# Kernel optimization log

Measured on AMD Instinct MI355X. Metric: run time of the kernel, lower is better.

## Reference

```python
import jax, jax.numpy as jnp
import numpy as np

H, QP, VP, D, DP = 4, 4, 4, 128, 64
DH = D // H


def setup_inputs() -> dict:
    key = jax.random.key(0)
    ks = jax.random.split(key, 16)
    B, L = 1, 1024
    w_c0 = float(np.log(np.e - 1.0))
    inp = {
        'single': jax.random.normal(ks[0], (B, L, D), jnp.float32),
        'pair': jax.random.normal(ks[1], (B, L, L, DP), jnp.float32),
        'T': jax.random.normal(ks[2], (B, L, 4, 4), jnp.float32),
        'w_C': jnp.full((H,), w_c0, jnp.float32),
        'ln_g': jnp.ones((D,), jnp.float32),
        'ln_b': jnp.zeros((D,), jnp.float32),
        'Wq': jax.random.normal(ks[3], (D, H * DH), jnp.float32) * 0.05,
        'Wk': jax.random.normal(ks[4], (D, H * DH), jnp.float32) * 0.05,
        'Wv': jax.random.normal(ks[5], (D, H * DH), jnp.float32) * 0.05,
        'Wqpt': jax.random.normal(ks[6], (D, H * QP * 3), jnp.float32) * 0.05,
        'Wkpt': jax.random.normal(ks[7], (D, H * QP * 3), jnp.float32) * 0.05,
        'Wvpt': jax.random.normal(ks[8], (D, H * VP * 3), jnp.float32) * 0.05,
        'Wb': jax.random.normal(ks[9], (DP, H), jnp.float32) * 0.05,
        'Wout': jax.random.normal(ks[10], (H * (DH + DP + VP * 3 + VP), D), jnp.float32) * 0.05,
        'b_out': jnp.zeros((D,), jnp.float32),
    }
    return inp


def _layernorm(x, g, b, eps=1e-5):
    x32 = x.astype(jnp.float32)
    mu = x32.mean(-1, keepdims=True)
    var = ((x32 - mu) ** 2).mean(-1, keepdims=True)
    return ((x32 - mu) * jax.lax.rsqrt(var + eps) * g + b).astype(x.dtype)


def reference(single, pair, T, w_C, ln_g, ln_b, Wq, Wk, Wv, Wqpt, Wkpt, Wvpt, Wb, Wout, b_out):
    B, L, Dm = single.shape
    scale_attn = DH ** (-0.5)
    z = _layernorm(single, ln_g, ln_b)
    Q = (z @ Wq).reshape(B, L, H, DH)
    K = (z @ Wk).reshape(B, L, H, DH)
    V = (z @ Wv).reshape(B, L, H, DH)
    Q_pt = (z @ Wqpt).reshape(B, L, H, QP, 3)
    K_pt = (z @ Wkpt).reshape(B, L, H, QP, 3)
    V_pt = (z @ Wvpt).reshape(B, L, H, VP, 3)
    R = T[..., :3, :3]   # [B,L,3,3]
    t = T[..., :3, 3]    # [B,L,3]
    # global-frame points: R @ p + t
    Q_g = jnp.einsum('blxy,blhpy->blhpx', R, Q_pt) + t[:, :, None, None, :]
    K_g = jnp.einsum('blxy,blhpy->blhpx', R, K_pt) + t[:, :, None, None, :]
    V_g = jnp.einsum('blxy,blhpy->blhpx', R, V_pt) + t[:, :, None, None, :]
    # scalar QK score [B,H,L,L]
    s_attn = jnp.einsum('bihd,bjhd->bhij', Q, K) * scale_attn
    # pair bias [B,H,L,L]
    b_attn = jnp.einsum('bijc,ch->bhij', pair, Wb)
    # squared point distance [B,H,L,L]
    diff = Q_g[:, :, None] - K_g[:, None]          # [B,L,L,H,QP,3]
    d2 = jnp.moveaxis((diff ** 2).sum((-1, -2)), -1, 1)
    w_pt = jax.nn.softplus(w_C)[None, :, None, None]
    attn = jax.nn.softmax(s_attn + b_attn - 0.5 * w_pt * d2, axis=-1)
    # scalar values [B,L,H*DH]
    o_s = jnp.einsum('bhij,bjhd->bihd', attn, V).reshape(B, L, H * DH)
    # point values aggregated in global frame then mapped back: R^T (p - t)
    o_pt_g = jnp.einsum('bhij,bjhpx->bihpx', attn, V_g)
    o_pt = jnp.einsum('blyx,blhpy->blhpx', R, o_pt_g - t[:, :, None, None, :])
    o_pt_n = jnp.sqrt((o_pt ** 2).sum(-1))
    # pair aggregation [B,L,H*DP]
    o_pair = jnp.einsum('bhij,bijc->bihc', attn, pair).reshape(B, L, H * DP)
    out = jnp.concatenate([o_s, o_pair, o_pt.reshape(B, L, -1), o_pt_n.reshape(B, L, -1)], axis=-1)
    return single + out @ Wout + b_out
```

## Files before the change

kernel.cpp:

```cpp
#include <hip/hip_runtime.h>
#include <math.h>

#define L_SEQ 1024
#define DM 128

#define OFF_KHAT 0
#define OFF_QHAT (L_SEQ * 192)
#define OFF_V    (OFF_QHAT + L_SEQ * 192)
#define OFF_VG   (OFF_V + L_SEQ * DM)

typedef __attribute__((address_space(1))) const void* gas_t;
typedef __attribute__((address_space(3))) void* las_t;

__device__ __forceinline__ void async16(const float4* g, float4* l) {
    __builtin_amdgcn_global_load_lds((gas_t)g, (las_t)l, 16, 0, 0);
}

__global__ __launch_bounds__(256) void ipa_prep(
    const float* __restrict__ single, const float* __restrict__ T,
    const float* __restrict__ w_C, const float* __restrict__ ln_g, const float* __restrict__ ln_b,
    const float* __restrict__ Wq, const float* __restrict__ Wk, const float* __restrict__ Wv,
    const float* __restrict__ Wqpt, const float* __restrict__ Wkpt, const float* __restrict__ Wvpt,
    float* __restrict__ ws)
{
    __shared__ float z_lds[128];
    __shared__ float proj[528];
    __shared__ float qg[4][4][3];
    __shared__ float kg[4][4][3];
    __shared__ float cq[4], ck[4];

    const int t = threadIdx.x;
    const int i = blockIdx.x;

    if (t < 64) {
        float x0 = single[i*DM + t];
        float x1 = single[i*DM + 64 + t];
        float s = x0 + x1, s2 = x0*x0 + x1*x1;
        #pragma unroll
        for (int off = 1; off < 64; off <<= 1) { s += __shfl_xor(s, off); s2 += __shfl_xor(s2, off); }
        float mu = s * 0.0078125f;
        float var = s2 * 0.0078125f - mu*mu;
        float rs = rsqrtf(var + 1e-5f);
        z_lds[t]      = (x0 - mu) * rs * ln_g[t]      + ln_b[t];
        z_lds[t + 64] = (x1 - mu) * rs * ln_g[t + 64] + ln_b[t + 64];
    }
    __syncthreads();

    for (int cc = t; cc < 528; cc += 256) {
        const float* W; int col, ncol;
        if (cc < 128)      { W = Wq;   col = cc;       ncol = 128; }
        else if (cc < 256) { W = Wk;   col = cc - 128; ncol = 128; }
        else if (cc < 384) { W = Wv;   col = cc - 256; ncol = 128; }
        else if (cc < 432) { W = Wqpt; col = cc - 384; ncol = 48;  }
        else if (cc < 480) { W = Wkpt; col = cc - 432; ncol = 48;  }
        else               { W = Wvpt; col = cc - 480; ncol = 48;  }
        float a = 0.f;
        #pragma unroll 8
        for (int k = 0; k < 128; ++k)
            a = fmaf(z_lds[k], W[k*ncol + col], a);
        proj[cc] = a;
    }
    __syncthreads();

    if (t < 16) {
        int h = t >> 2, p = t & 3;
        float R[3][3], tt[3];
        #pragma unroll
        for (int x = 0; x < 3; ++x) {
            #pragma unroll
            for (int y = 0; y < 3; ++y) R[x][y] = T[i*16 + x*4 + y];
            tt[x] = T[i*16 + x*4 + 3];
        }
        int base = 384 + (h*4 + p)*3;
        float q0 = proj[base],    q1 = proj[base+1],  q2 = proj[base+2];
        float k0 = proj[base+48], k1 = proj[base+49], k2 = proj[base+50];
        float v0 = proj[base+96], v1 = proj[base+97], v2 = proj[base+98];
        #pragma unroll
        for (int x = 0; x < 3; ++x) {
            float qq = R[x][0]*q0 + R[x][1]*q1 + R[x][2]*q2 + tt[x];
            float kk = R[x][0]*k0 + R[x][1]*k1 + R[x][2]*k2 + tt[x];
            float vv = R[x][0]*v0 + R[x][1]*v1 + R[x][2]*v2 + tt[x];
            qg[h][p][x] = qq;
            kg[h][p][x] = kk;
            ws[OFF_VG + (size_t)i*48 + h*12 + p*3 + x] = vv;
        }
    }
    __syncthreads();

    if (t < 8) {
        int h = t >> 1, isk = t & 1;
        float w = w_C[h];
        float wp = log1pf(__expf(w));
        float sq = 0.f;
        #pragma unroll
        for (int p = 0; p < 4; ++p)
            #pragma unroll
            for (int x = 0; x < 3; ++x) {
                float g = isk ? kg[h][p][x] : qg[h][p][x];
                sq += g*g;
            }
        float c = -0.5f * wp * sq;
        if (isk) ck[h] = c; else cq[h] = c;
    }
    __syncthreads();

    if (t < 128) ws[OFF_V + (size_t)i*DM + t] = proj[256 + t];
    const float scale_attn = 0.17677669529663687f;
    if (t < 192) {
        int h = t / 48, k = t % 48;
        float w = w_C[h];
        float wp = log1pf(__expf(w));
        float kv, qv;
        if (k < 32) {
            kv = proj[128 + h*32 + k];
            qv = scale_attn * proj[h*32 + k];
        } else if (k < 44) {
            int e = k - 32;
            kv = kg[h][e/3][e%3];
            qv = wp * qg[h][e/3][e%3];
        } else if (k == 44) { kv = ck[h]; qv = 1.0f; }
        else if (k == 45)   { kv = 1.0f; qv = cq[h]; }
        else                { kv = 0.f;  qv = 0.f; }
        ws[OFF_KHAT + (size_t)i*192 + t] = kv;
        ws[OFF_QHAT + (size_t)i*192 + t] = qv;
    }
}

__global__ __launch_bounds__(256, 2) void ipa_attn(
    const float* __restrict__ single, const float* __restrict__ pair,
    const float* __restrict__ T, const float* __restrict__ Wb,
    const float* __restrict__ Wout, const float* __restrict__ b_out,
    const float* __restrict__ ws, float* __restrict__ out)
{
    __shared__ __align__(16) float4 pair_w[4][2][16][16];
    __shared__ __align__(16) float4 qhat_lds[4][13];
    __shared__ __align__(16) float wbt_lds[4][68];
    __shared__ __align__(16) float p_ws[4][16][4];

    const int t = threadIdx.x;
    const int wv = t >> 6, lane = t & 63;
    const int i = blockIdx.x;

    if (t < 48) {
        int h = t / 12, k4 = t % 12;
        qhat_lds[h][k4] = ((const float4*)(ws + OFF_QHAT))[(size_t)i*48 + t];
    } else if (t < 112) {
        int c = t - 48;
        float4 w4 = ((const float4*)Wb)[c];
        wbt_lds[0][c] = w4.x; wbt_lds[1][c] = w4.y; wbt_lds[2][c] = w4.z; wbt_lds[3][c] = w4.w;
    }

    const int m_h  = lane & 3,  m_j  = lane >> 2;
    const int os_h = lane >> 4, os_jh = (lane >> 3) & 1, os_d4 = lane & 7;
    const int op_c4 = lane & 15, op_jq = lane >> 4;
    const int og_he = lane & 15, og_jq = lane >> 4;
    const bool og_act = og_he < 12;
    const int og_h  = (og_act ? og_he : 0) / 3;
    const int og_ix = og_act ? og_he : 0;

    float m_run = -INFINITY, l_run = 0.f;
    float4 accp[4];
    float4 accs = make_float4(0.f,0.f,0.f,0.f);
    float4 accg = make_float4(0.f,0.f,0.f,0.f);
    #pragma unroll
    for (int h = 0; h < 4; ++h) accp[h] = make_float4(0.f,0.f,0.f,0.f);

    const float4* pair4 = (const float4*)pair;
    const float4* kh4   = (const float4*)(ws + OFF_KHAT);
    const float4* v4    = (const float4*)(ws + OFF_V);
    const float4* vg4   = (const float4*)(ws + OFF_VG);
    float4* mypair = &pair_w[wv][0][0][0];
    const size_t prow_base = (size_t)i*L_SEQ + wv*256;

    #pragma unroll
    for (int it = 0; it < 4; ++it) {
        int idx = it*64 + lane;
        int j = idx >> 4, slot = idx & 15;
        int c4 = slot ^ (j & 7);
        async16(pair4 + (prow_base + j)*16 + c4, mypair + idx);
    }
    __syncthreads();

    for (int s = 0; s < 16; ++s) {
        const int cur = s & 1;
        const int j0 = wv*256 + s*16;

        float4 kh[12];
        {
            const float4* kp = kh4 + (size_t)(j0 + m_j)*48 + m_h*12;
            #pragma unroll
            for (int k4 = 0; k4 < 12; ++k4) kh[k4] = kp[k4];
        }
        if (s + 1 < 16) {
            #pragma unroll
            for (int it = 0; it < 4; ++it) {
                int idx = it*64 + lane;
                int j = idx >> 4, slot = idx & 15;
                int c4 = slot ^ (j & 7);
                async16(pair4 + (prow_base + (s+1)*16 + j)*16 + c4,
                        mypair + (1 - cur)*256 + idx);
            }
            asm volatile("s_waitcnt vmcnt(16)" ::: "memory");
        } else {
            asm volatile("s_waitcnt vmcnt(12)" ::: "memory");
        }

        const float4* prow = mypair + cur*256 + m_j*16;
        const float4* wrow = (const float4*)&wbt_lds[m_h][0];
        float bias = 0.f;
        #pragma unroll
        for (int cc = 0; cc < 16; ++cc) {
            int sw = cc ^ (m_j & 7);
            float4 pv = prow[sw];
            float4 wh = wrow[cc];
            bias += pv.x*wh.x + pv.y*wh.y + pv.z*wh.z + pv.w*wh.w;
        }
        float da = 0.f, db = 0.f;
        #pragma unroll
        for (int k4 = 0; k4 < 12; k4 += 2) {
            float4 qa = qhat_lds[m_h][k4], qb = qhat_lds[m_h][k4+1];
            da = fmaf(kh[k4].x,   qa.x, da); da = fmaf(kh[k4].y,   qa.y, da);
            da = fmaf(kh[k4].z,   qa.z, da); da = fmaf(kh[k4].w,   qa.w, da);
            db = fmaf(kh[k4+1].x, qb.x, db); db = fmaf(kh[k4+1].y, qb.y, db);
            db = fmaf(kh[k4+1].z, qb.z, db); db = fmaf(kh[k4+1].w, qb.w, db);
        }
        float logit = da + db + bias;

        float cmax = logit;
        cmax = fmaxf(cmax, __shfl_xor(cmax, 4));
        cmax = fmaxf(cmax, __shfl_xor(cmax, 8));
        cmax = fmaxf(cmax, __shfl_xor(cmax, 16));
        cmax = fmaxf(cmax, __shfl_xor(cmax, 32));
        float mn = fmaxf(m_run, cmax);
        float alpha = __expf(m_run - mn);
        float p = __expf(logit - mn);
        l_run = l_run * alpha + p;
        m_run = mn;
        p_ws[wv][m_j][m_h] = p;
        float a0 = __shfl(alpha, 0), a1 = __shfl(alpha, 1);
        float a2 = __shfl(alpha, 2), a3 = __shfl(alpha, 3);
        asm volatile("" ::: "memory");

        accp[0].x *= a0; accp[0].y *= a0; accp[0].z *= a0; accp[0].w *= a0;
        accp[1].x *= a1; accp[1].y *= a1; accp[1].z *= a1; accp[1].w *= a1;
        accp[2].x *= a2; accp[2].y *= a2; accp[2].z *= a2; accp[2].w *= a2;
        accp[3].x *= a3; accp[3].y *= a3; accp[3].z *= a3; accp[3].w *= a3;
        float aa_s = (os_h & 2) ? ((os_h & 1) ? a3 : a2) : ((os_h & 1) ? a1 : a0);
        float aa_g = (og_h & 2) ? ((og_h & 1) ? a3 : a2) : ((og_h & 1) ? a1 : a0);
        accs.x *= aa_s; accs.y *= aa_s; accs.z *= aa_s; accs.w *= aa_s;
        accg.x *= aa_g; accg.y *= aa_g; accg.z *= aa_g; accg.w *= aa_g;

        #pragma unroll
        for (int jj = 0; jj < 4; ++jj) {
            int j = op_jq*4 + jj;
            int sw = op_c4 ^ (j & 7);
            float4 pv = mypair[cur*256 + j*16 + sw];
            float4 pj = *(const float4*)&p_ws[wv][j][0];
            accp[0].x = fmaf(pj.x, pv.x, accp[0].x); accp[0].y = fmaf(pj.x, pv.y, accp[0].y);
            accp[0].z = fmaf(pj.x, pv.z, accp[0].z); accp[0].w = fmaf(pj.x, pv.w, accp[0].w);
            accp[1].x = fmaf(pj.y, pv.x, accp[1].x); accp[1].y = fmaf(pj.y, pv.y, accp[1].y);
            accp[1].z = fmaf(pj.y, pv.z, accp[1].z); accp[1].w = fmaf(pj.y, pv.w, accp[1].w);
            accp[2].x = fmaf(pj.z, pv.x, accp[2].x); accp[2].y = fmaf(pj.z, pv.y, accp[2].y);
            accp[2].z = fmaf(pj.z, pv.z, accp[2].z); accp[2].w = fmaf(pj.z, pv.w, accp[2].w);
            accp[3].x = fmaf(pj.w, pv.x, accp[3].x); accp[3].y = fmaf(pj.w, pv.y, accp[3].y);
            accp[3].z = fmaf(pj.w, pv.z, accp[3].z); accp[3].w = fmaf(pj.w, pv.w, accp[3].w);
        }
        #pragma unroll
        for (int jj = 0; jj < 8; ++jj) {
            int j = os_jh*8 + jj;
            float4 vvv = v4[(size_t)(j0 + j)*32 + os_h*8 + os_d4];
            float pa = p_ws[wv][j][os_h];
            accs.x = fmaf(pa, vvv.x, accs.x); accs.y = fmaf(pa, vvv.y, accs.y);
            accs.z = fmaf(pa, vvv.z, accs.z); accs.w = fmaf(pa, vvv.w, accs.w);
        }
        #pragma unroll
        for (int jj = 0; jj < 4; ++jj) {
            int j = og_jq*4 + jj;
            float4 gv = vg4[(size_t)(j0 + j)*12 + og_ix];
            float pa = og_act ? p_ws[wv][j][og_h] : 0.f;
            accg.x = fmaf(pa, gv.x, accg.x); accg.y = fmaf(pa, gv.y, accg.y);
            accg.z = fmaf(pa, gv.z, accg.z); accg.w = fmaf(pa, gv.w, accg.w);
        }
    }

    l_run += __shfl_xor(l_run, 4);  l_run += __shfl_xor(l_run, 8);
    l_run += __shfl_xor(l_run, 16); l_run += __shfl_xor(l_run, 32);
    #pragma unroll
    for (int h = 0; h < 4; ++h) {
        #pragma unroll
        for (int off = 16; off < 64; off <<= 1) {
            accp[h].x += __shfl_xor(accp[h].x, off);
            accp[h].y += __shfl_xor(accp[h].y, off);
            accp[h].z += __shfl_xor(accp[h].z, off);
            accp[h].w += __shfl_xor(accp[h].w, off);
        }
    }
    accs.x += __shfl_xor(accs.x, 8); accs.y += __shfl_xor(accs.y, 8);
    accs.z += __shfl_xor(accs.z, 8); accs.w += __shfl_xor(accs.w, 8);
    #pragma unroll
    for (int off = 16; off < 64; off <<= 1) {
        accg.x += __shfl_xor(accg.x, off); accg.y += __shfl_xor(accg.y, off);
        accg.z += __shfl_xor(accg.z, off); accg.w += __shfl_xor(accg.w, off);
    }

    float* scratch = (float*)&pair_w[0][0][0][0];
    float* cw = scratch + wv*2048;
    if (lane < 16) {
        #pragma unroll
        for (int h = 0; h < 4; ++h)
            *(float4*)&cw[h*64 + op_c4*4] = accp[h];
    }
    if (os_jh == 0) *(float4*)&cw[256 + os_h*32 + os_d4*4] = accs;
    if (lane < 12)  *(float4*)&cw[384 + lane*4] = accg;
    if (lane < 4)   { cw[432 + lane] = l_run; cw[436 + lane] = m_run; }
    __syncthreads();

    float* u    = scratch + 1024;
    float* og   = scratch + 1536;
    float* tmp  = scratch + 1600;
    float* wtS  = scratch + 1728;
    float* invS = scratch + 1744;

    if (t < 4) {
        int h = t;
        float m0 = scratch[436 + h],        m1 = scratch[2048 + 436 + h];
        float m2 = scratch[4096 + 436 + h], m3 = scratch[6144 + 436 + h];
        float M = fmaxf(fmaxf(m0, m1), fmaxf(m2, m3));
        float w0 = __expf(m0 - M), w1 = __expf(m1 - M);
        float w2 = __expf(m2 - M), w3 = __expf(m3 - M);
        float L = scratch[432+h]*w0 + scratch[2048+432+h]*w1
                + scratch[4096+432+h]*w2 + scratch[6144+432+h]*w3;
        wtS[h] = w0; wtS[4+h] = w1; wtS[8+h] = w2; wtS[12+h] = w3;
        invS[h] = 1.f / L;
    }
    __syncthreads();

    {
        int hp = t >> 6;
        float sum = scratch[t]*wtS[hp] + scratch[2048+t]*wtS[4+hp]
                  + scratch[4096+t]*wtS[8+hp] + scratch[6144+t]*wtS[12+hp];
        u[128 + t] = sum * invS[hp];
        if (t < 128) {
            int hs = t >> 5;
            float ssum = scratch[256+t]*wtS[hs] + scratch[2048+256+t]*wtS[4+hs]
                       + scratch[4096+256+t]*wtS[8+hs] + scratch[6144+256+t]*wtS[12+hs];
            u[t] = ssum * invS[hs];
        }
        if (t < 48) {
            int hg = t / 12;
            float gsum = scratch[384+t]*wtS[hg] + scratch[2048+384+t]*wtS[4+hg]
                       + scratch[4096+384+t]*wtS[8+hg] + scratch[6144+384+t]*wtS[12+hg];
            og[t] = gsum * invS[hg];
        }
    }
    __syncthreads();

    if (t < 16) {
        int h = t >> 2, p = t & 3;
        float R[3][3], tt[3];
        #pragma unroll
        for (int x = 0; x < 3; ++x) {
            #pragma unroll
            for (int y = 0; y < 3; ++y) R[x][y] = T[i*16 + x*4 + y];
            tt[x] = T[i*16 + x*4 + 3];
        }
        float v0 = og[h*12 + p*3+0] - tt[0];
        float v1 = og[h*12 + p*3+1] - tt[1];
        float v2 = og[h*12 + p*3+2] - tt[2];
        float n2 = 0.f;
        #pragma unroll
        for (int x = 0; x < 3; ++x) {
            float o = R[0][x]*v0 + R[1][x]*v1 + R[2][x]*v2;
            u[384 + h*12 + p*3 + x] = o;
            n2 += o*o;
        }
        u[432 + h*4 + p] = sqrtf(n2);
    }
    __syncthreads();

    {
        int d = t & 127, khf = t >> 7;
        float acc = 0.f;
        const float4* u4 = (const float4*)u;
        int k0 = khf * 56;
        #pragma unroll 4
        for (int k4 = k0; k4 < k0 + 56; ++k4) {
            float4 uu = u4[k4];
            const float* wp = Wout + (size_t)(k4*4)*128 + d;
            acc = fmaf(uu.x, wp[0],   acc);
            acc = fmaf(uu.y, wp[128], acc);
            acc = fmaf(uu.z, wp[256], acc);
            acc = fmaf(uu.w, wp[384], acc);
        }
        if (khf) tmp[d] = acc;
        __syncthreads();
        if (!khf) out[i*DM + d] = single[i*DM + d] + b_out[d] + acc + tmp[d];
    }
}

extern "C" void kernel_launch(void* const* d_in, const int* in_sizes, int n_in,
                              void* d_out, int out_size, void* d_ws, size_t ws_size,
                              hipStream_t stream)
{
    const float* single = (const float*)d_in[0];
    const float* pair   = (const float*)d_in[1];
    const float* T      = (const float*)d_in[2];
    const float* w_C    = (const float*)d_in[3];
    const float* ln_g   = (const float*)d_in[4];
    const float* ln_b   = (const float*)d_in[5];
    const float* Wq     = (const float*)d_in[6];
    const float* Wk     = (const float*)d_in[7];
    const float* Wv     = (const float*)d_in[8];
    const float* Wqpt   = (const float*)d_in[9];
    const float* Wkpt   = (const float*)d_in[10];
    const float* Wvpt   = (const float*)d_in[11];
    const float* Wb     = (const float*)d_in[12];
    const float* Wout   = (const float*)d_in[13];
    const float* b_out  = (const float*)d_in[14];
    float* out = (float*)d_out;
    float* ws  = (float*)d_ws;

    ipa_prep<<<1024, 256, 0, stream>>>(single, T, w_C, ln_g, ln_b, Wq, Wk, Wv, Wqpt, Wkpt, Wvpt, ws);
    ipa_attn<<<1024, 256, 0, stream>>>(single, pair, T, Wb, Wout, b_out, ws, out);
}
```

Measured before the change: 491.9 us.

## Process two query rows per attention block to reuse K, V and point-value loads

```diff
diff --git a/kernel.cpp b/kernel.cpp
--- a/kernel.cpp
+++ b/kernel.cpp
@@ -132,20 +132,20 @@
     const float* __restrict__ Wout, const float* __restrict__ b_out,
     const float* __restrict__ ws, float* __restrict__ out)
 {
-    __shared__ __align__(16) float4 pair_w[4][2][16][16];
-    __shared__ __align__(16) float4 qhat_lds[4][13];
+    __shared__ __align__(16) float4 pair_w[4][2][2][16][16];
+    __shared__ __align__(16) float4 qhat_lds[2][4][13];
     __shared__ __align__(16) float wbt_lds[4][68];
-    __shared__ __align__(16) float p_ws[4][16][4];
+    __shared__ __align__(16) float p_ws[4][2][16][4];
 
     const int t = threadIdx.x;
     const int wv = t >> 6, lane = t & 63;
-    const int i = blockIdx.x;
-
-    if (t < 48) {
-        int h = t / 12, k4 = t % 12;
-        qhat_lds[h][k4] = ((const float4*)(ws + OFF_QHAT))[(size_t)i*48 + t];
-    } else if (t < 112) {
-        int c = t - 48;
+    const int i0 = blockIdx.x * 2;
+
+    if (t < 96) {
+        int r = t / 48, rest = t % 48;
+        qhat_lds[r][rest/12][rest%12] = ((const float4*)(ws + OFF_QHAT))[(size_t)(i0+r)*48 + rest];
+    } else if (t < 160) {
+        int c = t - 96;
         float4 w4 = ((const float4*)Wb)[c];
         wbt_lds[0][c] = w4.x; wbt_lds[1][c] = w4.y; wbt_lds[2][c] = w4.z; wbt_lds[3][c] = w4.w;
     }
@@ -158,26 +158,30 @@
     const int og_h  = (og_act ? og_he : 0) / 3;
     const int og_ix = og_act ? og_he : 0;
 
-    float m_run = -INFINITY, l_run = 0.f;
-    float4 accp[4];
-    float4 accs = make_float4(0.f,0.f,0.f,0.f);
-    float4 accg = make_float4(0.f,0.f,0.f,0.f);
+    float m0_run = -INFINITY, l0_run = 0.f;
+    float m1_run = -INFINITY, l1_run = 0.f;
+    float4 accp[2][4];
+    float4 accs[2], accg[2];
     #pragma unroll
-    for (int h = 0; h < 4; ++h) accp[h] = make_float4(0.f,0.f,0.f,0.f);
+    for (int r = 0; r < 2; ++r) {
+        accs[r] = make_float4(0.f,0.f,0.f,0.f);
+        accg[r] = make_float4(0.f,0.f,0.f,0.f);
+        #pragma unroll
+        for (int h = 0; h < 4; ++h) accp[r][h] = make_float4(0.f,0.f,0.f,0.f);
+    }
 
     const float4* pair4 = (const float4*)pair;
     const float4* kh4   = (const float4*)(ws + OFF_KHAT);
     const float4* v4    = (const float4*)(ws + OFF_V);
     const float4* vg4   = (const float4*)(ws + OFF_VG);
-    float4* mypair = &pair_w[wv][0][0][0];
-    const size_t prow_base = (size_t)i*L_SEQ + wv*256;
+    float4* mypair = &pair_w[wv][0][0][0][0];
 
     #pragma unroll
-    for (int it = 0; it < 4; ++it) {
+    for (int it = 0; it < 8; ++it) {
         int idx = it*64 + lane;
-        int j = idx >> 4, slot = idx & 15;
+        int row = idx >> 8, j = (idx >> 4) & 15, slot = idx & 15;
         int c4 = slot ^ (j & 7);
-        async16(pair4 + (prow_base + j)*16 + c4, mypair + idx);
+        async16(pair4 + ((size_t)(i0+row)*L_SEQ + wv*256 + j)*16 + c4, mypair + idx);
     }
     __syncthreads();
 
@@ -191,200 +195,262 @@
             #pragma unroll
             for (int k4 = 0; k4 < 12; ++k4) kh[k4] = kp[k4];
         }
+        float4 vv[8];
+        #pragma unroll
+        for (int jj = 0; jj < 8; ++jj)
+            vv[jj] = v4[(size_t)(j0 + os_jh*8 + jj)*32 + os_h*8 + os_d4];
+        float4 gvv[4];
+        #pragma unroll
+        for (int jj = 0; jj < 4; ++jj)
+            gvv[jj] = vg4[(size_t)(j0 + og_jq*4 + jj)*12 + og_ix];
+
         if (s + 1 < 16) {
             #pragma unroll
-            for (int it = 0; it < 4; ++it) {
+            for (int it = 0; it < 8; ++it) {
                 int idx = it*64 + lane;
-                int j = idx >> 4, slot = idx & 15;
+                int row = idx >> 8, j = (idx >> 4) & 15, slot = idx & 15;
                 int c4 = slot ^ (j & 7);
-                async16(pair4 + (prow_base + (s+1)*16 + j)*16 + c4,
-                        mypair + (1 - cur)*256 + idx);
+                async16(pair4 + ((size_t)(i0+row)*L_SEQ + wv*256 + (s+1)*16 + j)*16 + c4,
+                        mypair + (1 - cur)*512 + idx);
             }
-            asm volatile("s_waitcnt vmcnt(16)" ::: "memory");
+            asm volatile("s_waitcnt vmcnt(32)" ::: "memory");
         } else {
-            asm volatile("s_waitcnt vmcnt(12)" ::: "memory");
-        }
-
-        const float4* prow = mypair + cur*256 + m_j*16;
-        const float4* wrow = (const float4*)&wbt_lds[m_h][0];
-        float bias = 0.f;
+            asm volatile("s_waitcnt vmcnt(24)" ::: "memory");
+        }
+
+        const float4* prow0 = mypair + cur*512 +       m_j*16;
+        const float4* prow1 = mypair + cur*512 + 256 + m_j*16;
+        const float4* wrow  = (const float4*)&wbt_lds[m_h][0];
+        float b0 = 0.f, b1 = 0.f;
         #pragma unroll
         for (int cc = 0; cc < 16; ++cc) {
             int sw = cc ^ (m_j & 7);
-            float4 pv = prow[sw];
-            float4 wh = wrow[cc];
-            bias += pv.x*wh.x + pv.y*wh.y + pv.z*wh.z + pv.w*wh.w;
-        }
-        float da = 0.f, db = 0.f;
+            float4 wh  = wrow[cc];
+            float4 pv0 = prow0[sw];
+            float4 pv1 = prow1[sw];
+            b0 += pv0.x*wh.x + pv0.y*wh.y + pv0.z*wh.z + pv0.w*wh.w;
+            b1 += pv1.x*wh.x + pv1.y*wh.y + pv1.z*wh.z + pv1.w*wh.w;
+        }
+        float d0a=0.f, d0b=0.f, d1a=0.f, d1b=0.f;
         #pragma unroll
         for (int k4 = 0; k4 < 12; k4 += 2) {
-            float4 qa = qhat_lds[m_h][k4], qb = qhat_lds[m_h][k4+1];
-            da = fmaf(kh[k4].x,   qa.x, da); da = fmaf(kh[k4].y,   qa.y, da);
-            da = fmaf(kh[k4].z,   qa.z, da); da = fmaf(kh[k4].w,   qa.w, da);
-            db = fmaf(kh[k4+1].x, qb.x, db); db = fmaf(kh[k4+1].y, qb.y, db);
-            db = fmaf(kh[k4+1].z, qb.z, db); db = fmaf(kh[k4+1].w, qb.w, db);
-        }
-        float logit = da + db + bias;
-
-        float cmax = logit;
-        cmax = fmaxf(cmax, __shfl_xor(cmax, 4));
-        cmax = fmaxf(cmax, __shfl_xor(cmax, 8));
-        cmax = fmaxf(cmax, __shfl_xor(cmax, 16));
-        cmax = fmaxf(cmax, __shfl_xor(cmax, 32));
-        float mn = fmaxf(m_run, cmax);
-        float alpha = __expf(m_run - mn);
-        float p = __expf(logit - mn);
-        l_run = l_run * alpha + p;
-        m_run = mn;
-        p_ws[wv][m_j][m_h] = p;
-        float a0 = __shfl(alpha, 0), a1 = __shfl(alpha, 1);
-        float a2 = __shfl(alpha, 2), a3 = __shfl(alpha, 3);
+            float4 q0a = qhat_lds[0][m_h][k4], q0b = qhat_lds[0][m_h][k4+1];
+            float4 q1a = qhat_lds[1][m_h][k4], q1b = qhat_lds[1][m_h][k4+1];
+            float4 ka = kh[k4], kb = kh[k4+1];
+            d0a = fmaf(ka.x, q0a.x, d0a); d0a = fmaf(ka.y, q0a.y, d0a);
+            d0a = fmaf(ka.z, q0a.z, d0a); d0a = fmaf(ka.w, q0a.w, d0a);
+            d0b = fmaf(kb.x, q0b.x, d0b); d0b = fmaf(kb.y, q0b.y, d0b);
+            d0b = fmaf(kb.z, q0b.z, d0b); d0b = fmaf(kb.w, q0b.w, d0b);
+            d1a = fmaf(ka.x, q1a.x, d1a); d1a = fmaf(ka.y, q1a.y, d1a);
+            d1a = fmaf(ka.z, q1a.z, d1a); d1a = fmaf(ka.w, q1a.w, d1a);
+            d1b = fmaf(kb.x, q1b.x, d1b); d1b = fmaf(kb.y, q1b.y, d1b);
+            d1b = fmaf(kb.z, q1b.z, d1b); d1b = fmaf(kb.w, q1b.w, d1b);
+        }
+        float logit0 = d0a + d0b + b0;
+        float logit1 = d1a + d1b + b1;
+
+        float c0 = logit0, c1 = logit1;
+        #pragma unroll
+        for (int off = 4; off < 64; off <<= 1) {
+            c0 = fmaxf(c0, __shfl_xor(c0, off));
+            c1 = fmaxf(c1, __shfl_xor(c1, off));
+        }
+        float mn0 = fmaxf(m0_run, c0), mn1 = fmaxf(m1_run, c1);
+        float al0 = __expf(m0_run - mn0), al1 = __expf(m1_run - mn1);
+        float p0 = __expf(logit0 - mn0), p1 = __expf(logit1 - mn1);
+        l0_run = l0_run * al0 + p0;  l1_run = l1_run * al1 + p1;
+        m0_run = mn0;  m1_run = mn1;
+        p_ws[wv][0][m_j][m_h] = p0;
+        p_ws[wv][1][m_j][m_h] = p1;
+        float a00 = __shfl(al0, 0), a01 = __shfl(al0, 1), a02 = __shfl(al0, 2), a03 = __shfl(al0, 3);
+        float a10 = __shfl(al1, 0), a11 = __shfl(al1, 1), a12 = __shfl(al1, 2), a13 = __shfl(al1, 3);
         asm volatile("" ::: "memory");
 
-        accp[0].x *= a0; accp[0].y *= a0; accp[0].z *= a0; accp[0].w *= a0;
-        accp[1].x *= a1; accp[1].y *= a1; accp[1].z *= a1; accp[1].w *= a1;
-        accp[2].x *= a2; accp[2].y *= a2; accp[2].z *= a2; accp[2].w *= a2;
-        accp[3].x *= a3; accp[3].y *= a3; accp[3].z *= a3; accp[3].w *= a3;
-        float aa_s = (os_h & 2) ? ((os_h & 1) ? a3 : a2) : ((os_h & 1) ? a1 : a0);
-        float aa_g = (og_h & 2) ? ((og_h & 1) ? a3 : a2) : ((og_h & 1) ? a1 : a0);
-        accs.x *= aa_s; accs.y *= aa_s; accs.z *= aa_s; accs.w *= aa_s;
-        accg.x *= aa_g; accg.y *= aa_g; accg.z *= aa_g; accg.w *= aa_g;
+        accp[0][0].x *= a00; accp[0][0].y *= a00; accp[0][0].z *= a00; accp[0][0].w *= a00;
+        accp[0][1].x *= a01; accp[0][1].y *= a01; accp[0][1].z *= a01; accp[0][1].w *= a01;
+        accp[0][2].x *= a02; accp[0][2].y *= a02; accp[0][2].z *= a02; accp[0][2].w *= a02;
+        accp[0][3].x *= a03; accp[0][3].y *= a03; accp[0][3].z *= a03; accp[0][3].w *= a03;
+        accp[1][0].x *= a10; accp[1][0].y *= a10; accp[1][0].z *= a10; accp[1][0].w *= a10;
+        accp[1][1].x *= a11; accp[1][1].y *= a11; accp[1][1].z *= a11; accp[1][1].w *= a11;
+        accp[1][2].x *= a12; accp[1][2].y *= a12; accp[1][2].z *= a12; accp[1][2].w *= a12;
+        accp[1][3].x *= a13; accp[1][3].y *= a13; accp[1][3].z *= a13; accp[1][3].w *= a13;
+        float as0 = (os_h & 2) ? ((os_h & 1) ? a03 : a02) : ((os_h & 1) ? a01 : a00);
+        float as1 = (os_h & 2) ? ((os_h & 1) ? a13 : a12) : ((os_h & 1) ? a11 : a10);
+        float ag0 = (og_h & 2) ? ((og_h & 1) ? a03 : a02) : ((og_h & 1) ? a01 : a00);
+        float ag1 = (og_h & 2) ? ((og_h & 1) ? a13 : a12) : ((og_h & 1) ? a11 : a10);
+        accs[0].x *= as0; accs[0].y *= as0; accs[0].z *= as0; accs[0].w *= as0;
+        accs[1].x *= as1; accs[1].y *= as1; accs[1].z *= as1; accs[1].w *= as1;
+        accg[0].x *= ag0; accg[0].y *= ag0; accg[0].z *= ag0; accg[0].w *= ag0;
+        accg[1].x *= ag1; accg[1].y *= ag1; accg[1].z *= ag1; accg[1].w *= ag1;
 
         #pragma unroll
         for (int jj = 0; jj < 4; ++jj) {
             int j = op_jq*4 + jj;
             int sw = op_c4 ^ (j & 7);
-            float4 pv = mypair[cur*256 + j*16 + sw];
-            float4 pj = *(const float4*)&p_ws[wv][j][0];
-            accp[0].x = fmaf(pj.x, pv.x, accp[0].x); accp[0].y = fmaf(pj.x, pv.y, accp[0].y);
-            accp[0].z = fmaf(pj.x, pv.z, accp[0].z); accp[0].w = fmaf(pj.x, pv.w, accp[0].w);
-            accp[1].x = fmaf(pj.y, pv.x, accp[1].x); accp[1].y = fmaf(pj.y, pv.y, accp[1].y);
-            accp[1].z = fmaf(pj.y, pv.z, accp[1].z); accp[1].w = fmaf(pj.y, pv.w, accp[1].w);
-            accp[2].x = fmaf(pj.z, pv.x, accp[2].x); accp[2].y = fmaf(pj.z, pv.y, accp[2].y);
-            accp[2].z = fmaf(pj.z, pv.z, accp[2].z); accp[2].w = fmaf(pj.z, pv.w, accp[2].w);
-            accp[3].x = fmaf(pj.w, pv.x, accp[3].x); accp[3].y = fmaf(pj.w, pv.y, accp[3].y);
-            accp[3].z = fmaf(pj.w, pv.z, accp[3].z); accp[3].w = fmaf(pj.w, pv.w, accp[3].w);
+            float4 pv0 = mypair[cur*512 +       j*16 + sw];
+            float4 pv1 = mypair[cur*512 + 256 + j*16 + sw];
+            float4 pj0 = *(const float4*)&p_ws[wv][0][j][0];
+            float4 pj1 = *(const float4*)&p_ws[wv][1][j][0];
+            accp[0][0].x = fmaf(pj0.x, pv0.x, accp[0][0].x); accp[0][0].y = fmaf(pj0.x, pv0.y, accp[0][0].y);
+            accp[0][0].z = fmaf(pj0.x, pv0.z, accp[0][0].z); accp[0][0].w = fmaf(pj0.x, pv0.w, accp[0][0].w);
+            accp[0][1].x = fmaf(pj0.y, pv0.x, accp[0][1].x); accp[0][1].y = fmaf(pj0.y, pv0.y, accp[0][1].y);
+            accp[0][1].z = fmaf(pj0.y, pv0.z, accp[0][1].z); accp[0][1].w = fmaf(pj0.y, pv0.w, accp[0][1].w);
+            accp[0][2].x = fmaf(pj0.z, pv0.x, accp[0][2].x); accp[0][2].y = fmaf(pj0.z, pv0.y, accp[0][2].y);
+            accp[0][2].z = fmaf(pj0.z, pv0.z, accp[0][2].z); accp[0][2].w = fmaf(pj0.z, pv0.w, accp[0][2].w);
+            accp[0][3].x = fmaf(pj0.w, pv0.x, accp[0][3].x); accp[0][3].y = fmaf(pj0.w, pv0.y, accp[0][3].y);
+            accp[0][3].z = fmaf(pj0.w, pv0.z, accp[0][3].z); accp[0][3].w = fmaf(pj0.w, pv0.w, accp[0][3].w);
+            accp[1][0].x = fmaf(pj1.x, pv1.x, accp[1][0].x); accp[1][0].y = fmaf(pj1.x, pv1.y, accp[1][0].y);
+            accp[1][0].z = fmaf(pj1.x, pv1.z, accp[1][0].z); accp[1][0].w = fmaf(pj1.x, pv1.w, accp[1][0].w);
+            accp[1][1].x = fmaf(pj1.y, pv1.x, accp[1][1].x); accp[1][1].y = fmaf(pj1.y, pv1.y, accp[1][1].y);
+            accp[1][1].z = fmaf(pj1.y, pv1.z, accp[1][1].z); accp[1][1].w = fmaf(pj1.y, pv1.w, accp[1][1].w);
+            accp[1][2].x = fmaf(pj1.z, pv1.x, accp[1][2].x); accp[1][2].y = fmaf(pj1.z, pv1.y, accp[1][2].y);
+            accp[1][2].z = fmaf(pj1.z, pv1.z, accp[1][2].z); accp[1][2].w = fmaf(pj1.z, pv1.w, accp[1][2].w);
+            accp[1][3].x = fmaf(pj1.w, pv1.x, accp[1][3].x); accp[1][3].y = fmaf(pj1.w, pv1.y, accp[1][3].y);
+            accp[1][3].z = fmaf(pj1.w, pv1.z, accp[1][3].z); accp[1][3].w = fmaf(pj1.w, pv1.w, accp[1][3].w);
         }
         #pragma unroll
         for (int jj = 0; jj < 8; ++jj) {
             int j = os_jh*8 + jj;
-            float4 vvv = v4[(size_t)(j0 + j)*32 + os_h*8 + os_d4];
-            float pa = p_ws[wv][j][os_h];
-            accs.x = fmaf(pa, vvv.x, accs.x); accs.y = fmaf(pa, vvv.y, accs.y);
-            accs.z = fmaf(pa, vvv.z, accs.z); accs.w = fmaf(pa, vvv.w, accs.w);
+            float pa0 = p_ws[wv][0][j][os_h];
+            float pa1 = p_ws[wv][1][j][os_h];
+            accs[0].x = fmaf(pa0, vv[jj].x, accs[0].x); accs[0].y = fmaf(pa0, vv[jj].y, accs[0].y);
+            accs[0].z = fmaf(pa0, vv[jj].z, accs[0].z); accs[0].w = fmaf(pa0, vv[jj].w, accs[0].w);
+            accs[1].x = fmaf(pa1, vv[jj].x, accs[1].x); accs[1].y = fmaf(pa1, vv[jj].y, accs[1].y);
+            accs[1].z = fmaf(pa1, vv[jj].z, accs[1].z); accs[1].w = fmaf(pa1, vv[jj].w, accs[1].w);
         }
         #pragma unroll
         for (int jj = 0; jj < 4; ++jj) {
             int j = og_jq*4 + jj;
-            float4 gv = vg4[(size_t)(j0 + j)*12 + og_ix];
-            float pa = og_act ? p_ws[wv][j][og_h] : 0.f;
-            accg.x = fmaf(pa, gv.x, accg.x); accg.y = fmaf(pa, gv.y, accg.y);
-            accg.z = fmaf(pa, gv.z, accg.z); accg.w = fmaf(pa, gv.w, accg.w);
-        }
-    }
-
-    l_run += __shfl_xor(l_run, 4);  l_run += __shfl_xor(l_run, 8);
-    l_run += __shfl_xor(l_run, 16); l_run += __shfl_xor(l_run, 32);
+            float pg0 = og_act ? p_ws[wv][0][j][og_h] : 0.f;
+            float pg1 = og_act ? p_ws[wv][1][j][og_h] : 0.f;
+            accg[0].x = fmaf(pg0, gvv[jj].x, accg[0].x); accg[0].y = fmaf(pg0, gvv[jj].y, accg[0].y);
+            accg[0].z = fmaf(pg0, gvv[jj].z, accg[0].z); accg[0].w = fmaf(pg0, gvv[jj].w, accg[0].w);
+            accg[1].x = fmaf(pg1, gvv[jj].x, accg[1].x); accg[1].y = fmaf(pg1, gvv[jj].y, accg[1].y);
+            accg[1].z = fmaf(pg1, gvv[jj].z, accg[1].z); accg[1].w = fmaf(pg1, gvv[jj].w, accg[1].w);
+        }
+    }
+
     #pragma unroll
-    for (int h = 0; h < 4; ++h) {
+    for (int off = 4; off < 64; off <<= 1) { l0_run += __shfl_xor(l0_run, off); l1_run += __shfl_xor(l1_run, off); }
+    #pragma unroll
+    for (int r = 0; r < 2; ++r) {
+        #pragma unroll
+        for (int h = 0; h < 4; ++h) {
+            #pragma unroll
+            for (int off = 16; off < 64; off <<= 1) {
+                accp[r][h].x += __shfl_xor(accp[r][h].x, off);
+                accp[r][h].y += __shfl_xor(accp[r][h].y, off);
+                accp[r][h].z += __shfl_xor(accp[r][h].z, off);
+                accp[r][h].w += __shfl_xor(accp[r][h].w, off);
+            }
+        }
+        accs[r].x += __shfl_xor(accs[r].x, 8); accs[r].y += __shfl_xor(accs[r].y, 8);
+        accs[r].z += __shfl_xor(accs[r].z, 8); accs[r].w += __shfl_xor(accs[r].w, 8);
         #pragma unroll
         for (int off = 16; off < 64; off <<= 1) {
-            accp[h].x += __shfl_xor(accp[h].x, off);
-            accp[h].y += __shfl_xor(accp[h].y, off);
-            accp[h].z += __shfl_xor(accp[h].z, off);
-            accp[h].w += __shfl_xor(accp[h].w, off);
-        }
-    }
-    accs.x += __shfl_xor(accs.x, 8); accs.y += __shfl_xor(accs.y, 8);
-    accs.z += __shfl_xor(accs.z, 8); accs.w += __shfl_xor(accs.w, 8);
+            accg[r].x += __shfl_xor(accg[r].x, off); accg[r].y += __shfl_xor(accg[r].y, off);
+            accg[r].z += __shfl_xor(accg[r].z, off); accg[r].w += __shfl_xor(accg[r].w, off);
+        }
+    }
+
+    float* scratch = (float*)&pair_w[0][0][0][0][0];
+    float* cw = scratch + wv*4096;
     #pragma unroll
-    for (int off = 16; off < 64; off <<= 1) {
-        accg.x += __shfl_xor(accg.x, off); accg.y += __shfl_xor(accg.y, off);
-        accg.z += __shfl_xor(accg.z, off); accg.w += __shfl_xor(accg.w, off);
-    }
-
-    float* scratch = (float*)&pair_w[0][0][0][0];
-    float* cw = scratch + wv*2048;
-    if (lane < 16) {
-        #pragma unroll
-        for (int h = 0; h < 4; ++h)
-            *(float4*)&cw[h*64 + op_c4*4] = accp[h];
-    }
-    if (os_jh == 0) *(float4*)&cw[256 + os_h*32 + os_d4*4] = accs;
-    if (lane < 12)  *(float4*)&cw[384 + lane*4] = accg;
-    if (lane < 4)   { cw[432 + lane] = l_run; cw[436 + lane] = m_run; }
-    __syncthreads();
-
-    float* u    = scratch + 1024;
-    float* og   = scratch + 1536;
-    float* tmp  = scratch + 1600;
-    float* wtS  = scratch + 1728;
-    float* invS = scratch + 1744;
-
-    if (t < 4) {
-        int h = t;
-        float m0 = scratch[436 + h],        m1 = scratch[2048 + 436 + h];
-        float m2 = scratch[4096 + 436 + h], m3 = scratch[6144 + 436 + h];
+    for (int r = 0; r < 2; ++r) {
+        if (lane < 16) {
+            #pragma unroll
+            for (int h = 0; h < 4; ++h)
+                *(float4*)&cw[r*512 + h*64 + op_c4*4] = accp[r][h];
+        }
+        if (os_jh == 0) *(float4*)&cw[r*512 + 256 + os_h*32 + os_d4*4] = accs[r];
+        if (lane < 12)  *(float4*)&cw[r*512 + 384 + lane*4] = accg[r];
+        if (lane < 4) {
+            cw[r*512 + 432 + m_h] = (r == 0) ? l0_run : l1_run;
+            cw[r*512 + 436 + m_h] = (r == 0) ? m0_run : m1_run;
+        }
+    }
+    __syncthreads();
+
+    const int EP = 1024;
+    float* u   = scratch + EP;
+    float* og2 = scratch + EP + 896;
+    float* wts = scratch + EP + 992;
+    float* ivs = scratch + EP + 1024;
+
+    if (t < 8) {
+        int r = t >> 2, h = t & 3;
+        float m0 = scratch[0*4096 + r*512 + 436 + h], m1 = scratch[1*4096 + r*512 + 436 + h];
+        float m2 = scratch[2*4096 + r*512 + 436 + h], m3 = scratch[3*4096 + r*512 + 436 + h];
         float M = fmaxf(fmaxf(m0, m1), fmaxf(m2, m3));
         float w0 = __expf(m0 - M), w1 = __expf(m1 - M);
         float w2 = __expf(m2 - M), w3 = __expf(m3 - M);
-        float L = scratch[432+h]*w0 + scratch[2048+432+h]*w1
-                + scratch[4096+432+h]*w2 + scratch[6144+432+h]*w3;
-        wtS[h] = w0; wtS[4+h] = w1; wtS[8+h] = w2; wtS[12+h] = w3;
-        invS[h] = 1.f / L;
+        float L = scratch[0*4096 + r*512 + 432 + h]*w0 + scratch[1*4096 + r*512 + 432 + h]*w1
+                + scratch[2*4096 + r*512 + 432 + h]*w2 + scratch[3*4096 + r*512 + 432 + h]*w3;
+        wts[r*16 + 0 + h] = w0; wts[r*16 + 4 + h] = w1;
+        wts[r*16 + 8 + h] = w2; wts[r*16 + 12 + h] = w3;
+        ivs[r*4 + h] = 1.f / L;
     }
     __syncthreads();
 
     {
-        int hp = t >> 6;
-        float sum = scratch[t]*wtS[hp] + scratch[2048+t]*wtS[4+hp]
-                  + scratch[4096+t]*wtS[8+hp] + scratch[6144+t]*wtS[12+hp];
-        u[128 + t] = sum * invS[hp];
-        if (t < 128) {
-            int hs = t >> 5;
-            float ssum = scratch[256+t]*wtS[hs] + scratch[2048+256+t]*wtS[4+hs]
-                       + scratch[4096+256+t]*wtS[8+hs] + scratch[6144+256+t]*wtS[12+hs];
-            u[t] = ssum * invS[hs];
-        }
-        if (t < 48) {
-            int hg = t / 12;
-            float gsum = scratch[384+t]*wtS[hg] + scratch[2048+384+t]*wtS[4+hg]
-                       + scratch[4096+384+t]*wtS[8+hg] + scratch[6144+384+t]*wtS[12+hg];
-            og[t] = gsum * invS[hg];
-        }
-    }
-    __syncthreads();
-
-    if (t < 16) {
-        int h = t >> 2, p = t & 3;
+        int r = t >> 7, q = t & 127;
+        const float* wt = wts + r*16;
+        const float* iv = ivs + r*4;
+        {
+            int hs = q >> 5;
+            float v = scratch[0*4096 + r*512 + 256 + q]*wt[0 + hs] + scratch[1*4096 + r*512 + 256 + q]*wt[4 + hs]
+                    + scratch[2*4096 + r*512 + 256 + q]*wt[8 + hs] + scratch[3*4096 + r*512 + 256 + q]*wt[12 + hs];
+            u[r*448 + q] = v * iv[hs];
+        }
+        #pragma unroll
+        for (int pp = 0; pp < 2; ++pp) {
+            int idx = pp*128 + q;
+            int hp = idx >> 6;
+            float v = scratch[0*4096 + r*512 + idx]*wt[0 + hp] + scratch[1*4096 + r*512 + idx]*wt[4 + hp]
+                    + scratch[2*4096 + r*512 + idx]*wt[8 + hp] + scratch[3*4096 + r*512 + idx]*wt[12 + hp];
+            u[r*448 + 128 + idx] = v * iv[hp];
+        }
+        if (t < 96) {
+            int r2 = t / 48, qg = t % 48, hg = qg / 12;
+            const float* wt2 = wts + r2*16;
+            float v = scratch[0*4096 + r2*512 + 384 + qg]*wt2[0 + hg] + scratch[1*4096 + r2*512 + 384 + qg]*wt2[4 + hg]
+                    + scratch[2*4096 + r2*512 + 384 + qg]*wt2[8 + hg] + scratch[3*4096 + r2*512 + 384 + qg]*wt2[12 + hg];
+            og2[r2*48 + qg] = v * ivs[r2*4 + hg];
+        }
+    }
+    __syncthreads();
+
+    if (t < 32) {
+        int r = t >> 4, idx = t & 15, h = idx >> 2, p = idx & 3;
+        int ii = i0 + r;
         float R[3][3], tt[3];
         #pragma unroll
         for (int x = 0; x < 3; ++x) {
             #pragma unroll
-            for (int y = 0; y < 3; ++y) R[x][y] = T[i*16 + x*4 + y];
-            tt[x] = T[i*16 + x*4 + 3];
-        }
-        float v0 = og[h*12 + p*3+0] - tt[0];
-        float v1 = og[h*12 + p*3+1] - tt[1];
-        float v2 = og[h*12 + p*3+2] - tt[2];
+            for (int y = 0; y < 3; ++y) R[x][y] = T[ii*16 + x*4 + y];
+            tt[x] = T[ii*16 + x*4 + 3];
+        }
+        float v0 = og2[r*48 + h*12 + p*3+0] - tt[0];
+        float v1 = og2[r*48 + h*12 + p*3+1] - tt[1];
+        float v2 = og2[r*48 + h*12 + p*3+2] - tt[2];
         float n2 = 0.f;
         #pragma unroll
         for (int x = 0; x < 3; ++x) {
             float o = R[0][x]*v0 + R[1][x]*v1 + R[2][x]*v2;
-            u[384 + h*12 + p*3 + x] = o;
+            u[r*448 + 384 + h*12 + p*3 + x] = o;
             n2 += o*o;
         }
-        u[432 + h*4 + p] = sqrtf(n2);
+        u[r*448 + 432 + h*4 + p] = sqrtf(n2);
     }
     __syncthreads();
 
     {
-        int d = t & 127, khf = t >> 7;
-        float acc = 0.f;
-        const float4* u4 = (const float4*)u;
-        int k0 = khf * 56;
+        int r = t >> 7, d = t & 127;
+        int ii = i0 + r;
+        float acc = single[ii*DM + d] + b_out[d];
+        const float4* u4 = (const float4*)(u + r*448);
         #pragma unroll 4
-        for (int k4 = k0; k4 < k0 + 56; ++k4) {
+        for (int k4 = 0; k4 < 112; ++k4) {
             float4 uu = u4[k4];
             const float* wp = Wout + (size_t)(k4*4)*128 + d;
             acc = fmaf(uu.x, wp[0],   acc);
@@ -392,9 +458,7 @@
             acc = fmaf(uu.z, wp[256], acc);
             acc = fmaf(uu.w, wp[384], acc);
         }
-        if (khf) tmp[d] = acc;
-        __syncthreads();
-        if (!khf) out[i*DM + d] = single[i*DM + d] + b_out[d] + acc + tmp[d];
+        out[ii*DM + d] = acc;
     }
 }
 
@@ -421,5 +485,5 @@
     float* ws  = (float*)d_ws;
 
     ipa_prep<<<1024, 256, 0, stream>>>(single, T, w_C, ln_g, ln_b, Wq, Wk, Wv, Wqpt, Wkpt, Wvpt, ws);
-    ipa_attn<<<1024, 256, 0, stream>>>(single, pair, T, Wb, Wout, b_out, ws, out);
+    ipa_attn<<<512, 256, 0, stream>>>(single, pair, T, Wb, Wout, b_out, ws, out);
 }
```

Result: slower. 519.9 us (+5.7%).
